# Performance work log

Measured on AMD Instinct MI355X. Metric: run time of the kernel, lower is better.

## Reference

```python
import jax, jax.numpy as jnp
import numpy as np

N, D = 32, 16  # output capsules, output capsule dim
J, I = 16, 8   # input capsules, input capsule dim
B = 16384

def setup_inputs() -> dict:
    key = jax.random.key(0)
    k1, k2 = jax.random.split(key)
    inputs = jax.random.normal(k1, (B, J, I), dtype=jnp.float32)
    # kaiming_normal_ on (N,16,8,D): fan_in computed from dims -> std = sqrt(2/fan_in)
    fan_in = I * D  # torch fan_in for a 4D tensor (N,16,8,D) is dim1*receptive? faithful scale: gain*sqrt(1/fan)
    W = jax.random.normal(k2, (N, J, I, D), dtype=jnp.float32) * np.float32(np.sqrt(2.0 / (J * I * D / N if False else fan_in)))
    b = jnp.zeros((N, J, 1), dtype=jnp.float32)
    return {"inputs": inputs, "W": W, "b": b}

def reference(inputs, W, b):
    # pose transform: u[b,n,j,z] = sum_i inputs[b,j,i] * W[n,j,i,z]
    u = jnp.einsum('bji,njiz->bnjz', inputs, W)          # (B, N, J, D)
    # self-agreement: c[b,n,i] = sum_{k,j} u[b,n,i,j] * u[b,n,k,j]
    c = jnp.einsum('bnij,bnj->bni', u, u.sum(axis=-2))   # (B, N, J)
    c = c[..., None] / jnp.sqrt(jnp.float32(D))          # (B, N, J, 1)
    c = jax.nn.softmax(c, axis=1)                        # softmax over N axis (torch dim=1)
    c = c + b                                            # broadcast (N, J, 1)
    s = jnp.sum(u * c, axis=-2)                          # (B, N, D)
    return s
```

## Files before the change

### kernel.cpp

```cpp
#include <hip/hip_runtime.h>

#define B_TOT 16384
#define TBB   16
#define NTH   256
#define SLS   524

typedef short bf16x8 __attribute__((ext_vector_type(8)));
typedef float f32x4  __attribute__((ext_vector_type(4)));

__device__ __forceinline__ unsigned int f2bf(float f) {
    unsigned int u = __float_as_uint(f);
    return (u + 0x7fffu + ((u >> 16) & 1u)) >> 16;
}

__global__ void prepack_W(const float* __restrict__ W, uint4* __restrict__ Wp)
{
    const int t  = blockIdx.x * 256 + threadIdx.x;
    const int z  = t & 15;
    const int nj = t >> 4;
    const float* src = W + (size_t)nj * 128 + z;
    uint4 o;
    o.x = f2bf(src[0])  | (f2bf(src[16])  << 16);
    o.y = f2bf(src[32]) | (f2bf(src[48])  << 16);
    o.z = f2bf(src[64]) | (f2bf(src[80])  << 16);
    o.w = f2bf(src[96]) | (f2bf(src[112]) << 16);
    Wp[t] = o;
}

__global__ __launch_bounds__(NTH, 3)
void caps_mfma(const float* __restrict__ X,
               const uint4*  __restrict__ Wp,
               const float* __restrict__ Bias,
               float* __restrict__ Out)
{
    __shared__ __align__(16) float sL[TBB * SLS];
    __shared__ float sBias[512];

    const int t    = threadIdx.x;
    const int lane = t & 63;
    const int wv   = t >> 6;
    const int l16  = lane & 15;
    const int zg   = lane >> 4;
    const long bb  = (long)blockIdx.x * TBB;

    sBias[t]       = Bias[t];
    sBias[t + 256] = Bias[t + 256];

    union U8 { bf16x8 v; uint4 q; };
    bf16x8 xf[16];
    {
        U8 z8; z8.q = make_uint4(0u, 0u, 0u, 0u);
        #pragma unroll
        for (int j = 0; j < 16; ++j) xf[j] = z8.v;
    }
    if (lane < 16) {
        const float* xr = X + (bb + l16) * 128;
        #pragma unroll
        for (int j = 0; j < 16; ++j) {
            float4 a = *reinterpret_cast<const float4*>(xr + j * 8);
            float4 b = *reinterpret_cast<const float4*>(xr + j * 8 + 4);
            U8 p;
            p.q.x = f2bf(a.x) | (f2bf(a.y) << 16);
            p.q.y = f2bf(a.z) | (f2bf(a.w) << 16);
            p.q.z = f2bf(b.x) | (f2bf(b.y) << 16);
            p.q.w = f2bf(b.z) | (f2bf(b.w) << 16);
            xf[j] = p.v;
        }
    }

    const f32x4 zero4 = {0.f, 0.f, 0.f, 0.f};

    #pragma unroll 1
    for (int q = 0; q < 8; ++q) {
        const int n = wv * 8 + q;
        const uint4* wpn = Wp + n * 256 + l16;

        f32x4 acc[4] = {zero4, zero4, zero4, zero4};
        #pragma unroll
        for (int j = 0; j < 16; ++j) {
            U8 a; a.q = wpn[j * 16];
            acc[j & 3] = __builtin_amdgcn_mfma_f32_16x16x32_bf16(a.v, xf[j], acc[j & 3], 0, 0, 0);
        }
        const f32x4 usum = (acc[0] + acc[1]) + (acc[2] + acc[3]);

        float lv[16];
        #pragma unroll
        for (int j = 0; j < 16; ++j) {
            U8 a; a.q = wpn[j * 16];
            f32x4 u = __builtin_amdgcn_mfma_f32_16x16x32_bf16(a.v, xf[j], zero4, 0, 0, 0);
            float p = u[0] * usum[0];
            p = fmaf(u[1], usum[1], p);
            p = fmaf(u[2], usum[2], p);
            p = fmaf(u[3], usum[3], p);
            p += __shfl_xor(p, 16);
            p += __shfl_xor(p, 32);
            lv[j] = p * 0.25f;
        }
        if (lane < 16) {
            float4* dst = reinterpret_cast<float4*>(&sL[l16 * SLS + n * 16]);
            dst[0] = make_float4(lv[0],  lv[1],  lv[2],  lv[3]);
            dst[1] = make_float4(lv[4],  lv[5],  lv[6],  lv[7]);
            dst[2] = make_float4(lv[8],  lv[9],  lv[10], lv[11]);
            dst[3] = make_float4(lv[12], lv[13], lv[14], lv[15]);
        }
    }
    __syncthreads();

    {
        const int sb = t >> 4, sj = t & 15;
        float l[32];
        #pragma unroll
        for (int n = 0; n < 32; ++n) l[n] = sL[sb * SLS + n * 16 + sj];
        float m = l[0];
        #pragma unroll
        for (int n = 1; n < 32; ++n) m = fmaxf(m, l[n]);
        float Z = 0.f;
        #pragma unroll
        for (int n = 0; n < 32; ++n) { l[n] = __expf(l[n] - m); Z += l[n]; }
        const float inv = 1.0f / Z;
        #pragma unroll
        for (int n = 0; n < 32; ++n)
            sL[sb * SLS + n * 16 + sj] = fmaf(l[n], inv, sBias[n * 16 + sj]);
    }
    __syncthreads();

    #pragma unroll 1
    for (int q = 0; q < 8; ++q) {
        const int n = wv * 8 + q;
        const uint4* wpn = Wp + n * 256 + l16;
        const float4* cp = reinterpret_cast<const float4*>(&sL[l16 * SLS + n * 16]);
        const float4 c0 = cp[0], c1 = cp[1], c2 = cp[2], c3 = cp[3];
        const float cj[16] = {c0.x,c0.y,c0.z,c0.w, c1.x,c1.y,c1.z,c1.w,
                              c2.x,c2.y,c2.z,c2.w, c3.x,c3.y,c3.z,c3.w};
        float s0 = 0.f, s1 = 0.f, s2 = 0.f, s3 = 0.f;
        #pragma unroll
        for (int j = 0; j < 16; ++j) {
            U8 a; a.q = wpn[j * 16];
            f32x4 u = __builtin_amdgcn_mfma_f32_16x16x32_bf16(a.v, xf[j], zero4, 0, 0, 0);
            s0 = fmaf(cj[j], u[0], s0);
            s1 = fmaf(cj[j], u[1], s1);
            s2 = fmaf(cj[j], u[2], s2);
            s3 = fmaf(cj[j], u[3], s3);
        }
        float4* op = reinterpret_cast<float4*>(Out + (bb + l16) * 512 + n * 16 + zg * 4);
        *op = make_float4(s0, s1, s2, s3);
    }
}

extern "C" void kernel_launch(void* const* d_in, const int* in_sizes, int n_in,
                              void* d_out, int out_size, void* d_ws, size_t ws_size,
                              hipStream_t stream) {
    const float* X  = (const float*)d_in[0];
    const float* W  = (const float*)d_in[1];
    const float* Bi = (const float*)d_in[2];
    float* Out = (float*)d_out;

    uint4* Wp = (uint4*)d_ws;
    prepack_W<<<32, 256, 0, stream>>>(W, Wp);
    caps_mfma<<<B_TOT / TBB, NTH, 0, stream>>>(X, Wp, Bi, Out);
}
```

Before: 118.1 us.

## Repack W and X across all MFMA lanes to fill the K dimension

```diff
diff --git a/kernel.cpp b/kernel.cpp
--- a/kernel.cpp
+++ b/kernel.cpp
@@ -7,31 +7,44 @@
 
 typedef short bf16x8 __attribute__((ext_vector_type(8)));
 typedef float f32x4  __attribute__((ext_vector_type(4)));
+union U4 { bf16x8 v; uint4 q; };
 
-__device__ __forceinline__ unsigned int f2bf(float f) {
-    unsigned int u = __float_as_uint(f);
+__device__ __forceinline__ unsigned f2bf(float f) {
+    unsigned u = __float_as_uint(f);
     return (u + 0x7fffu + ((u >> 16) & 1u)) >> 16;
 }
 
-__global__ void prepack_W(const float* __restrict__ W, uint4* __restrict__ Wp)
-{
-    const int t  = blockIdx.x * 256 + threadIdx.x;
-    const int z  = t & 15;
-    const int nj = t >> 4;
-    const float* src = W + (size_t)nj * 128 + z;
+__device__ __forceinline__ uint4 packrow(const float* src) {
     uint4 o;
     o.x = f2bf(src[0])  | (f2bf(src[16])  << 16);
     o.y = f2bf(src[32]) | (f2bf(src[48])  << 16);
     o.z = f2bf(src[64]) | (f2bf(src[80])  << 16);
     o.w = f2bf(src[96]) | (f2bf(src[112]) << 16);
-    Wp[t] = o;
+    return o;
 }
 
-__global__ __launch_bounds__(NTH, 3)
-void caps_mfma(const float* __restrict__ X,
-               const uint4*  __restrict__ Wp,
-               const float* __restrict__ Bias,
-               float* __restrict__ Out)
+__global__ void prepack(const float* __restrict__ W, uint4* __restrict__ Wp)
+{
+    const int t = blockIdx.x * 256 + threadIdx.x;
+    if (t < 8192) {
+        const int lane = t & 63, s = (t >> 6) & 3, n = t >> 8;
+        const int q = lane >> 4, z = lane & 15;
+        const int j = 4 * s + q;
+        Wp[t] = packrow(W + (size_t)(n * 16 + j) * 128 + z);
+    } else {
+        const int u = t - 8192;
+        const int lane = u & 63, j = (u >> 6) & 15, n = u >> 10;
+        const int q = lane >> 4, z = lane & 15;
+        uint4 o = make_uint4(0u, 0u, 0u, 0u);
+        if (q == (j & 3))
+            o = packrow(W + (size_t)(n * 16 + j) * 128 + z);
+        Wp[t] = o;
+    }
+}
+
+__global__ __launch_bounds__(NTH, 4)
+void caps(const float* __restrict__ X, const uint4* __restrict__ Wp,
+          const float* __restrict__ Bias, float* __restrict__ Out)
 {
     __shared__ __align__(16) float sL[TBB * SLS];
     __shared__ float sBias[512];
@@ -39,55 +52,49 @@
     const int t    = threadIdx.x;
     const int lane = t & 63;
     const int wv   = t >> 6;
-    const int l16  = lane & 15;
-    const int zg   = lane >> 4;
+    const int b16  = lane & 15;
+    const int q    = lane >> 4;
     const long bb  = (long)blockIdx.x * TBB;
 
     sBias[t]       = Bias[t];
     sBias[t + 256] = Bias[t + 256];
 
-    union U8 { bf16x8 v; uint4 q; };
-    bf16x8 xf[16];
-    {
-        U8 z8; z8.q = make_uint4(0u, 0u, 0u, 0u);
-        #pragma unroll
-        for (int j = 0; j < 16; ++j) xf[j] = z8.v;
-    }
-    if (lane < 16) {
-        const float* xr = X + (bb + l16) * 128;
-        #pragma unroll
-        for (int j = 0; j < 16; ++j) {
-            float4 a = *reinterpret_cast<const float4*>(xr + j * 8);
-            float4 b = *reinterpret_cast<const float4*>(xr + j * 8 + 4);
-            U8 p;
-            p.q.x = f2bf(a.x) | (f2bf(a.y) << 16);
-            p.q.y = f2bf(a.z) | (f2bf(a.w) << 16);
-            p.q.z = f2bf(b.x) | (f2bf(b.y) << 16);
-            p.q.w = f2bf(b.z) | (f2bf(b.w) << 16);
-            xf[j] = p.v;
-        }
+    uint4 xq[4];
+    #pragma unroll
+    for (int s = 0; s < 4; ++s) {
+        const float* xs = X + (bb + b16) * 128 + (4 * s + q) * 8;
+        float4 a = *reinterpret_cast<const float4*>(xs);
+        float4 c = *reinterpret_cast<const float4*>(xs + 4);
+        uint4 o;
+        o.x = f2bf(a.x) | (f2bf(a.y) << 16);
+        o.y = f2bf(a.z) | (f2bf(a.w) << 16);
+        o.z = f2bf(c.x) | (f2bf(c.y) << 16);
+        o.w = f2bf(c.z) | (f2bf(c.w) << 16);
+        xq[s] = o;
     }
 
     const f32x4 zero4 = {0.f, 0.f, 0.f, 0.f};
 
     #pragma unroll 1
-    for (int q = 0; q < 8; ++q) {
-        const int n = wv * 8 + q;
-        const uint4* wpn = Wp + n * 256 + l16;
+    for (int nq = 0; nq < 8; ++nq) {
+        const int n = wv * 8 + nq;
+        const uint4* wk = Wp + n * 256 + lane;
 
-        f32x4 acc[4] = {zero4, zero4, zero4, zero4};
+        f32x4 usum = zero4;
         #pragma unroll
-        for (int j = 0; j < 16; ++j) {
-            U8 a; a.q = wpn[j * 16];
-            acc[j & 3] = __builtin_amdgcn_mfma_f32_16x16x32_bf16(a.v, xf[j], acc[j & 3], 0, 0, 0);
+        for (int s = 0; s < 4; ++s) {
+            U4 a;  a.q  = wk[s * 64];
+            U4 xb; xb.q = xq[s];
+            usum = __builtin_amdgcn_mfma_f32_16x16x32_bf16(a.v, xb.v, usum, 0, 0, 0);
         }
-        const f32x4 usum = (acc[0] + acc[1]) + (acc[2] + acc[3]);
 
+        const uint4* wj = Wp + 8192 + n * 1024 + lane;
         float lv[16];
         #pragma unroll
         for (int j = 0; j < 16; ++j) {
-            U8 a; a.q = wpn[j * 16];
-            f32x4 u = __builtin_amdgcn_mfma_f32_16x16x32_bf16(a.v, xf[j], zero4, 0, 0, 0);
+            U4 a;  a.q  = wj[j * 64];
+            U4 xb; xb.q = xq[j >> 2];
+            f32x4 u = __builtin_amdgcn_mfma_f32_16x16x32_bf16(a.v, xb.v, zero4, 0, 0, 0);
             float p = u[0] * usum[0];
             p = fmaf(u[1], usum[1], p);
             p = fmaf(u[2], usum[2], p);
@@ -97,7 +104,7 @@
             lv[j] = p * 0.25f;
         }
         if (lane < 16) {
-            float4* dst = reinterpret_cast<float4*>(&sL[l16 * SLS + n * 16]);
+            float4* dst = reinterpret_cast<float4*>(&sL[b16 * SLS + n * 16]);
             dst[0] = make_float4(lv[0],  lv[1],  lv[2],  lv[3]);
             dst[1] = make_float4(lv[4],  lv[5],  lv[6],  lv[7]);
             dst[2] = make_float4(lv[8],  lv[9],  lv[10], lv[11]);
@@ -124,25 +131,25 @@
     }
     __syncthreads();
 
-    #pragma unroll 1
-    for (int q = 0; q < 8; ++q) {
-        const int n = wv * 8 + q;
-        const uint4* wpn = Wp + n * 256 + l16;
-        const float4* cp = reinterpret_cast<const float4*>(&sL[l16 * SLS + n * 16]);
-        const float4 c0 = cp[0], c1 = cp[1], c2 = cp[2], c3 = cp[3];
-        const float cj[16] = {c0.x,c0.y,c0.z,c0.w, c1.x,c1.y,c1.z,c1.w,
-                              c2.x,c2.y,c2.z,c2.w, c3.x,c3.y,c3.z,c3.w};
+    #pragma unroll 2
+    for (int nq = 0; nq < 8; ++nq) {
+        const int n = wv * 8 + nq;
+        const uint4* wj = Wp + 8192 + n * 1024 + lane;
         float s0 = 0.f, s1 = 0.f, s2 = 0.f, s3 = 0.f;
         #pragma unroll
-        for (int j = 0; j < 16; ++j) {
-            U8 a; a.q = wpn[j * 16];
-            f32x4 u = __builtin_amdgcn_mfma_f32_16x16x32_bf16(a.v, xf[j], zero4, 0, 0, 0);
-            s0 = fmaf(cj[j], u[0], s0);
-            s1 = fmaf(cj[j], u[1], s1);
-            s2 = fmaf(cj[j], u[2], s2);
-            s3 = fmaf(cj[j], u[3], s3);
+        for (int jp = 0; jp < 8; ++jp) {
+            float2 c2 = *reinterpret_cast<const float2*>(&sL[b16 * SLS + n * 16 + 2 * jp]);
+            U4 a0; a0.q = wj[(2 * jp) * 64];
+            U4 a1; a1.q = wj[(2 * jp + 1) * 64];
+            U4 x0; x0.q = xq[jp >> 1];
+            f32x4 u0 = __builtin_amdgcn_mfma_f32_16x16x32_bf16(a0.v, x0.v, zero4, 0, 0, 0);
+            f32x4 u1 = __builtin_amdgcn_mfma_f32_16x16x32_bf16(a1.v, x0.v, zero4, 0, 0, 0);
+            s0 = fmaf(c2.x, u0[0], s0); s0 = fmaf(c2.y, u1[0], s0);
+            s1 = fmaf(c2.x, u0[1], s1); s1 = fmaf(c2.y, u1[1], s1);
+            s2 = fmaf(c2.x, u0[2], s2); s2 = fmaf(c2.y, u1[2], s2);
+            s3 = fmaf(c2.x, u0[3], s3); s3 = fmaf(c2.y, u1[3], s3);
         }
-        float4* op = reinterpret_cast<float4*>(Out + (bb + l16) * 512 + n * 16 + zg * 4);
+        float4* op = reinterpret_cast<float4*>(Out + (bb + b16) * 512 + n * 16 + q * 4);
         *op = make_float4(s0, s1, s2, s3);
     }
 }
@@ -156,6 +163,6 @@
     float* Out = (float*)d_out;
 
     uint4* Wp = (uint4*)d_ws;
-    prepack_W<<<32, 256, 0, stream>>>(W, Wp);
-    caps_mfma<<<B_TOT / TBB, NTH, 0, stream>>>(X, Wp, Bi, Out);
+    prepack<<<160, 256, 0, stream>>>(W, Wp);
+    caps<<<B_TOT / TBB, NTH, 0, stream>>>(X, Wp, Bi, Out);
 }
```

Result: faster. 113.8 us (-3.6%).
